# Optimization experiments

Measured on AMD Instinct MI355X. Metric: run time of the kernel, lower is better.

Reference implementation:

```python
import jax, jax.numpy as jnp
import numpy as np

B, S, HID = 2, 2048, 2048
H, KV, D = 32, 4, 128
G = H // KV
EPS = 1e-6
SCALE = D ** -0.5
ROPE_THETA = 1000000.0


def setup_inputs() -> dict:
    key = jax.random.key(0)
    ks = jax.random.split(key, 6)
    hidden_states = jax.random.normal(ks[0], (B, S, HID), jnp.float32)
    # real RoPE tables (position_embeddings passed into forward)
    inv_freq = 1.0 / (ROPE_THETA ** (np.arange(0, D, 2, dtype=np.float32) / D))
    ang = np.arange(S, dtype=np.float32)[:, None] * inv_freq[None, :]  # [S, D/2]
    emb = np.concatenate([ang, ang], axis=-1)  # [S, D]
    cos = jnp.broadcast_to(jnp.asarray(np.cos(emb)), (B, S, D))
    sin = jnp.broadcast_to(jnp.asarray(np.sin(emb)), (B, S, D))
    sd = 0.02
    wq = jax.random.normal(ks[1], (H * D, HID), jnp.float32) * sd
    wk = jax.random.normal(ks[2], (KV * D, HID), jnp.float32) * sd
    wv = jax.random.normal(ks[3], (KV * D, HID), jnp.float32) * sd
    wo = jax.random.normal(ks[4], (HID, H * D), jnp.float32) * sd
    q_norm_w = jnp.ones((D,), jnp.float32)
    k_norm_w = jnp.ones((D,), jnp.float32)
    return {"hidden_states": hidden_states, "cos": cos, "sin": sin,
            "wq": wq, "wk": wk, "wv": wv, "wo": wo,
            "q_norm_w": q_norm_w, "k_norm_w": k_norm_w}


def _rms_norm(x, w):
    var = jnp.mean(jnp.square(x), axis=-1, keepdims=True)
    return x * jax.lax.rsqrt(var + EPS) * w


def _rotate_half(x):
    x1, x2 = jnp.split(x, 2, axis=-1)
    return jnp.concatenate([-x2, x1], axis=-1)


def _rope(x, cos, sin):
    # x: [B,S,N,D]; cos/sin: [B,S,1,D] (unsqueeze_dim=2)
    return x * cos + _rotate_half(x) * sin


def reference(hidden_states, cos, sin, wq, wk, wv, wo, q_norm_w, k_norm_w):
    x = hidden_states
    q = jnp.einsum('bsh,oh->bso', x, wq).reshape(B, S, H, D)
    k = jnp.einsum('bsh,oh->bso', x, wk).reshape(B, S, KV, D)
    v = jnp.einsum('bsh,oh->bso', x, wv).reshape(B, S, KV, D)
    q = _rms_norm(q, q_norm_w)
    k = _rms_norm(k, k_norm_w)
    c = cos[:, :, None, :]
    s = sin[:, :, None, :]
    q = _rope(q, c, s)
    k = _rope(k, c, s)
    # GQA causal attention, BSND layout
    qg = q.reshape(B, S, KV, G, D)
    scores = jnp.einsum('bqkgd,bskd->bkgqs', qg, k) * SCALE  # [B,KV,G,Sq,Sk]
    causal = jnp.tril(jnp.ones((S, S), bool))
    scores = jnp.where(causal, scores, jnp.finfo(scores.dtype).min)
    p = jax.nn.softmax(scores, axis=-1)
    out = jnp.einsum('bkgqs,bskd->bqkgd', p, v).reshape(B, S, H * D)
    return jnp.einsum('bso,ho->bsh', out, wo)
```

## Files before the change

### kernel.cpp

```cpp
#include <hip/hip_runtime.h>
#include <hip/hip_bf16.h>

typedef __attribute__((ext_vector_type(8))) short short8;
typedef __attribute__((ext_vector_type(4))) float f32x4;

#define DEVI static __device__ __forceinline__

constexpr int Bb = 2, Ss = 2048, Hh = 32, KVc = 4, Dc = 128;
constexpr float EPSc = 1e-6f;
constexpr float SCALEc = 0.08838834764831845f;

DEVI float bf2f(short s) {
  unsigned u = ((unsigned)(unsigned short)s) << 16;
  float f; __builtin_memcpy(&f, &u, 4); return f;
}
DEVI short f2bf(float f) {
  __hip_bfloat16 h = __float2bfloat16(f);
  unsigned short u; __builtin_memcpy(&u, &h, 2); return (short)u;
}

#define GLDS(gsrc, ldst) __builtin_amdgcn_global_load_lds( \
    (const __attribute__((address_space(1))) void*)(gsrc), \
    (__attribute__((address_space(3))) void*)(ldst), 16, 0, 0)

struct Cvt5 { const float* src[5]; short* dst[5]; };
__global__ void cvt_all(Cvt5 a) {
  constexpr int CUM[6] = {0, 2097152, 4194304, 4456448, 4718592, 6815744};
  const int stride = gridDim.x * blockDim.x;
  for (int i = blockIdx.x * blockDim.x + threadIdx.x; i < 6815744; i += stride) {
    int s = 0;
#pragma unroll
    for (int t = 1; t < 5; ++t) if (i >= CUM[t]) s = t;
    int j = i - CUM[s];
    float4 v = ((const float4*)a.src[s])[j];
    short4 o;
    o.x = f2bf(v.x); o.y = f2bf(v.y); o.z = f2bf(v.z); o.w = f2bf(v.w);
    ((short4*)a.dst[s])[j] = o;
  }
}

template<int MODE>
__launch_bounds__(256, 2)
__global__ void gemm_bt(const short* __restrict__ A,
                        const short* __restrict__ B0,
                        const short* __restrict__ B1,
                        const short* __restrict__ B2,
                        short* __restrict__ oq,
                        short* __restrict__ ok,
                        short* __restrict__ ov,
                        float* __restrict__ of,
                        const float* __restrict__ cosb,
                        const float* __restrict__ sinb,
                        const float* __restrict__ qnw,
                        const float* __restrict__ knw,
                        int K)
{
  __shared__ short lA[128 * 32];
  __shared__ short lB[128 * 32];
  const int tid = threadIdx.x;
  const int lane = tid & 63;
  const int wvi = tid >> 6;
  const int l15 = lane & 15, g = lane >> 4;
  const int m0 = blockIdx.x * 128;
  const int nt = blockIdx.y;
  const short* Bp; int n0, region;
  if (MODE == 0) {
    if (nt < 32)      { Bp = B0; n0 = nt * 128;        region = 0; }
    else if (nt < 36) { Bp = B1; n0 = (nt - 32) * 128; region = 1; }
    else              { Bp = B2; n0 = (nt - 36) * 128; region = 2; }
  } else { Bp = B0; n0 = nt * 128; region = 3; }

  const int wrow = wvi * 32;
  const int srow = tid >> 2, schunk = tid & 3;

  f32x4 acc[2][8] = {};

  for (int k0 = 0; k0 < K; k0 += 32) {
    __syncthreads();
#pragma unroll
    for (int c = 0; c < 2; ++c) {
      int row = c * 64 + srow;
      int gc = schunk ^ ((row >> 1) & 3);
      GLDS(A  + (size_t)(m0 + row) * K + k0 + gc * 8, lA + (c * 256 + tid) * 8);
      GLDS(Bp + (size_t)(n0 + row) * K + k0 + gc * 8, lB + (c * 256 + tid) * 8);
    }
    __syncthreads();
    short8 afr[2], bfr[8];
#pragma unroll
    for (int i = 0; i < 2; ++i) {
      int ra = wrow + i * 16 + l15;
      afr[i] = *(const short8*)(lA + ra * 32 + ((g ^ ((ra >> 1) & 3)) * 8));
    }
#pragma unroll
    for (int i = 0; i < 8; ++i) {
      int rb = i * 16 + l15;
      bfr[i] = *(const short8*)(lB + rb * 32 + ((g ^ ((rb >> 1) & 3)) * 8));
    }
#pragma unroll
    for (int mi = 0; mi < 2; ++mi)
#pragma unroll
      for (int ni = 0; ni < 8; ++ni)
        acc[mi][ni] = __builtin_amdgcn_mfma_f32_16x16x32_bf16(afr[mi], bfr[ni], acc[mi][ni], 0, 0, 0);
  }

  if (MODE == 1) {
#pragma unroll
    for (int mi = 0; mi < 2; ++mi)
#pragma unroll
      for (int r = 0; r < 4; ++r) {
        int m = m0 + wrow + mi * 16 + g * 4 + r;
#pragma unroll
        for (int ni = 0; ni < 8; ++ni)
          of[(size_t)m * 2048 + n0 + ni * 16 + l15] = acc[mi][ni][r];
      }
  } else if (region == 2) {
#pragma unroll
    for (int mi = 0; mi < 2; ++mi)
#pragma unroll
      for (int r = 0; r < 4; ++r) {
        int m = m0 + wrow + mi * 16 + g * 4 + r;
        int b = m >> 11, s = m & 2047;
#pragma unroll
        for (int ni = 0; ni < 8; ++ni) {
          int n = n0 + ni * 16 + l15;
          int kvi = n >> 7, d = n & 127;
          ov[(((size_t)b * KVc + kvi) * 128 + d) * Ss + s] = f2bf(acc[mi][ni][r]);
        }
      }
  } else {
    const float* wnorm = (region == 0) ? qnw : knw;
    float w8[8];
#pragma unroll
    for (int ni = 0; ni < 8; ++ni) w8[ni] = wnorm[ni * 16 + l15];
#pragma unroll
    for (int mi = 0; mi < 2; ++mi)
#pragma unroll
      for (int r = 0; r < 4; ++r) {
        int m = m0 + wrow + mi * 16 + g * 4 + r;
        int b = m >> 11, s = m & 2047;
        float xv[8];
        float ssq = 0.f;
#pragma unroll
        for (int ni = 0; ni < 8; ++ni) { xv[ni] = acc[mi][ni][r]; ssq += xv[ni] * xv[ni]; }
        ssq += __shfl_xor(ssq, 1);
        ssq += __shfl_xor(ssq, 2);
        ssq += __shfl_xor(ssq, 4);
        ssq += __shfl_xor(ssq, 8);
        float inv = rsqrtf(ssq * (1.0f / 128.0f) + EPSc);
        float xn[8];
#pragma unroll
        for (int ni = 0; ni < 8; ++ni) xn[ni] = xv[ni] * inv * w8[ni];
        const float* cpr = cosb + ((size_t)b * Ss + s) * Dc;
        const float* spr = sinb + ((size_t)b * Ss + s) * Dc;
#pragma unroll
        for (int ni = 0; ni < 8; ++ni) {
          int dl = ni * 16 + l15;
          float c = cpr[dl], sn = spr[dl];
          float rot = (ni < 4) ? -xn[ni + 4] : xn[ni - 4];
          float o = xn[ni] * c + rot * sn;
          int n = n0 + dl;
          if (region == 0) {
            oq[(size_t)m * 4096 + n] = f2bf(o * SCALEc);
          } else {
            int kvi = n >> 7, d = n & 127;
            ok[(((size_t)b * KVc + kvi) * Ss + s) * 128 + d] = f2bf(o);
          }
        }
      }
  }
}

__launch_bounds__(256, 2)
__global__ void attn_fwd(const short* __restrict__ qb,
                         const short* __restrict__ kbuf,
                         const short* __restrict__ vtbuf,
                         short* __restrict__ ob)
{
  __shared__ short lK[2][64 * 128];
  __shared__ short lV[2][128 * 64];
  __shared__ short lP[4][32 * 32];
  const int tid = threadIdx.x, lane = tid & 63, wvi = tid >> 6;
  const int l15 = lane & 15, g = lane >> 4;
  const int pi = blockIdx.x, h = blockIdx.y, b = blockIdx.z;
  const int kv = h >> 3;
  const short* kp = kbuf  + ((size_t)b * KVc + kv) * Ss * 128;
  const short* vp = vtbuf + ((size_t)b * KVc + kv) * 128 * Ss;
  const int krow = tid >> 4, kch = tid & 15;
  const int vrow = tid >> 3, vch = tid & 7;

  for (int which = 0; which < 2; ++which) {
    const int qt = which ? (15 - pi) : pi;
    const int qwb = qt * 128 + wvi * 32;
    const int nkt = 2 * qt + 2;

    short8 qf[2][4];
#pragma unroll
    for (int qs = 0; qs < 2; ++qs)
#pragma unroll
      for (int dc = 0; dc < 4; ++dc)
        qf[qs][dc] = *(const short8*)(qb + (size_t)(b * Ss + qwb + qs * 16 + l15) * 4096
                                         + h * 128 + dc * 32 + g * 8);

    f32x4 oacc[2][8] = {};
    float mrun[2] = { -__builtin_inff(), -__builtin_inff() };
    float lrun[2] = { 0.f, 0.f };

    auto STAGE = [&](int kt, int bufi) {
      const int kb0 = kt * 64;
#pragma unroll
      for (int c = 0; c < 4; ++c) {
        int r = c * 16 + krow;
        int gc = kch ^ (r & 7);
        GLDS(kp + (size_t)(kb0 + r) * 128 + gc * 8, &lK[bufi][(c * 256 + tid) * 8]);
      }
#pragma unroll
      for (int c = 0; c < 4; ++c) {
        int r = c * 32 + vrow;
        int gc = vch ^ (r & 7);
        GLDS(vp + (size_t)r * Ss + kb0 + gc * 8, &lV[bufi][(c * 256 + tid) * 8]);
      }
    };

    STAGE(0, 0);
    STAGE(1, 1);

    for (int kt = 0; kt < nkt; ++kt) {
      const int cb = kt & 1;
      if (kt + 1 < nkt) asm volatile("s_waitcnt vmcnt(8)" ::: "memory");
      else              asm volatile("s_waitcnt vmcnt(0)" ::: "memory");
      __builtin_amdgcn_s_barrier();
      asm volatile("" ::: "memory");

#pragma unroll
      for (int half = 0; half < 2; ++half) {
        const int kb0 = kt * 64 + half * 32;
        if (kb0 <= qwb + 31) {
          short8 kf[2][4];
#pragma unroll
          for (int ks = 0; ks < 2; ++ks)
#pragma unroll
            for (int dc = 0; dc < 4; ++dc) {
              int row = half * 32 + ks * 16 + l15;
              kf[ks][dc] = *(const short8*)(&lK[cb][0] + row * 128 + (((dc * 4 + g) ^ (row & 7)) * 8));
            }
          f32x4 st[2][2] = {};
          __builtin_amdgcn_s_setprio(1);
#pragma unroll
          for (int qs = 0; qs < 2; ++qs)
#pragma unroll
            for (int ks = 0; ks < 2; ++ks)
#pragma unroll
              for (int dc = 0; dc < 4; ++dc)
                st[qs][ks] = __builtin_amdgcn_mfma_f32_16x16x32_bf16(kf[ks][dc], qf[qs][dc], st[qs][ks], 0, 0, 0);
          __builtin_amdgcn_s_setprio(0);

          const bool need_mask = (kb0 + 31 > qwb);
#pragma unroll
          for (int qs = 0; qs < 2; ++qs) {
            const int qg = qwb + qs * 16 + l15;
            float p[8];
            float tmax = -__builtin_inff();
#pragma unroll
            for (int ks = 0; ks < 2; ++ks)
#pragma unroll
              for (int r = 0; r < 4; ++r) {
                float v = st[qs][ks][r];
                if (need_mask && (kb0 + ks * 16 + g * 4 + r > qg)) v = -__builtin_inff();
                p[ks * 4 + r] = v;
                tmax = fmaxf(tmax, v);
              }
            tmax = fmaxf(tmax, __shfl_xor(tmax, 16));
            tmax = fmaxf(tmax, __shfl_xor(tmax, 32));
            float m_use = mrun[qs];
            if (__any(tmax > m_use + 8.0f)) {
              float mnew = fmaxf(m_use, tmax);
              float scl = __expf(m_use - mnew);
              lrun[qs] *= scl;
              mrun[qs] = mnew;
#pragma unroll
              for (int r = 0; r < 4; ++r) {
                float sc = __shfl(scl, g * 4 + r);
#pragma unroll
                for (int dt = 0; dt < 8; ++dt)
                  oacc[qs][dt][r] *= sc;
              }
              m_use = mnew;
            }
            float rsum = 0.f;
#pragma unroll
            for (int j = 0; j < 8; ++j) { p[j] = __expf(p[j] - m_use); rsum += p[j]; }
            rsum += __shfl_xor(rsum, 16);
            rsum += __shfl_xor(rsum, 32);
            lrun[qs] += rsum;
            {
              int row = qs * 16 + l15;
              int sw = (row >> 1) & 3;
              short* pr = lP[wvi] + row * 32;
#pragma unroll
              for (int ks = 0; ks < 2; ++ks) {
                int idx = (((2 * ks + (g >> 1)) ^ sw) * 8) + (g & 1) * 4;
                short4 pw;
                pw.x = f2bf(p[ks * 4 + 0]);
                pw.y = f2bf(p[ks * 4 + 1]);
                pw.z = f2bf(p[ks * 4 + 2]);
                pw.w = f2bf(p[ks * 4 + 3]);
                *(short4*)(pr + idx) = pw;
              }
            }
          }
          asm volatile("" ::: "memory");
          short8 vf[8];
#pragma unroll
          for (int dt = 0; dt < 8; ++dt) {
            int row = dt * 16 + l15;
            vf[dt] = *(const short8*)(&lV[cb][0] + row * 64 + (((half * 4 + g) ^ (row & 7)) * 8));
          }
          __builtin_amdgcn_s_setprio(1);
#pragma unroll
          for (int qs = 0; qs < 2; ++qs) {
            int row = qs * 16 + l15;
            short8 pf = *(const short8*)(lP[wvi] + row * 32 + ((g ^ ((row >> 1) & 3)) * 8));
#pragma unroll
            for (int dt = 0; dt < 8; ++dt)
              oacc[qs][dt] = __builtin_amdgcn_mfma_f32_16x16x32_bf16(pf, vf[dt], oacc[qs][dt], 0, 0, 0);
          }
          __builtin_amdgcn_s_setprio(0);
          asm volatile("" ::: "memory");
        }
      }

      asm volatile("" ::: "memory");
      __builtin_amdgcn_s_barrier();
      if (kt + 2 < nkt) STAGE(kt + 2, cb);
    }

#pragma unroll
    for (int qs = 0; qs < 2; ++qs)
#pragma unroll
      for (int r = 0; r < 4; ++r) {
        float inv = 1.0f / __shfl(lrun[qs], g * 4 + r);
        int qrow = qwb + qs * 16 + g * 4 + r;
        short* op = ob + (size_t)(b * Ss + qrow) * 4096 + h * 128;
#pragma unroll
        for (int dt = 0; dt < 8; ++dt)
          op[dt * 16 + l15] = f2bf(oacc[qs][dt][r] * inv);
      }
  }
}

extern "C" void kernel_launch(void* const* d_in, const int* in_sizes, int n_in,
                              void* d_out, int out_size, void* d_ws, size_t ws_size,
                              hipStream_t stream) {
  const float* x    = (const float*)d_in[0];
  const float* cosb = (const float*)d_in[1];
  const float* sinb = (const float*)d_in[2];
  const float* wq   = (const float*)d_in[3];
  const float* wk   = (const float*)d_in[4];
  const float* wv   = (const float*)d_in[5];
  const float* wo   = (const float*)d_in[6];
  const float* qw   = (const float*)d_in[7];
  const float* kw   = (const float*)d_in[8];

  size_t off = 0;
  auto alloc = [&](size_t bytes) {
    char* p = (char*)d_ws + off;
    off += (bytes + 255) & ~(size_t)255;
    return p;
  };
  short* x_bf  = (short*)alloc((size_t)8388608 * 2);
  short* wq_bf = (short*)alloc((size_t)8388608 * 2);
  short* wk_bf = (short*)alloc((size_t)1048576 * 2);
  short* wv_bf = (short*)alloc((size_t)1048576 * 2);
  short* wo_bf = (short*)alloc((size_t)8388608 * 2);
  short* q_bf  = (short*)alloc((size_t)16777216 * 2);
  short* k_bf  = (short*)alloc((size_t)2097152 * 2);
  short* v_bf  = (short*)alloc((size_t)2097152 * 2);
  short* ao_bf = (short*)alloc((size_t)16777216 * 2);

  Cvt5 ca;
  ca.src[0] = x;    ca.dst[0] = x_bf;
  ca.src[1] = wq;   ca.dst[1] = wq_bf;
  ca.src[2] = wk;   ca.dst[2] = wk_bf;
  ca.src[3] = wv;   ca.dst[3] = wv_bf;
  ca.src[4] = wo;   ca.dst[4] = wo_bf;
  cvt_all<<<2048, 256, 0, stream>>>(ca);

  gemm_bt<0><<<dim3(32, 40), 256, 0, stream>>>(x_bf, wq_bf, wk_bf, wv_bf,
                                               q_bf, k_bf, v_bf, nullptr,
                                               cosb, sinb, qw, kw, 2048);
  attn_fwd<<<dim3(8, 32, 2), 256, 0, stream>>>(q_bf, k_bf, v_bf, ao_bf);
  gemm_bt<1><<<dim3(32, 16), 256, 0, stream>>>(ao_bf, wo_bf, nullptr, nullptr,
                                               nullptr, nullptr, nullptr, (float*)d_out,
                                               nullptr, nullptr, nullptr, nullptr, 4096);
}
```

Before: 355.0 us.

## Double-buffer GEMM LDS tiles with async global-to-LDS prefetch two stages ahead

The projection GEMM kernel now keeps two LDS buffers for the A and B tiles and issues global_load_lds for the next K-slices while MFMAs run on the current one. Explicit vmcnt waits and raw barriers replace the two __syncthreads per iteration, so load latency can overlap with compute. The launch-bounds occupancy hint also rises from 2 to 4 blocks, which doubles LDS use per block and may force register spills. The hand-written vmcnt counting is fragile if the compiler emits other vector memory operations inside the loop.

```diff
diff --git a/kernel.cpp b/kernel.cpp
--- a/kernel.cpp
+++ b/kernel.cpp
@@ -40,7 +40,7 @@
 }
 
 template<int MODE>
-__launch_bounds__(256, 2)
+__launch_bounds__(256, 4)
 __global__ void gemm_bt(const short* __restrict__ A,
                         const short* __restrict__ B0,
                         const short* __restrict__ B1,
@@ -55,8 +55,8 @@
                         const float* __restrict__ knw,
                         int K)
 {
-  __shared__ short lA[128 * 32];
-  __shared__ short lB[128 * 32];
+  __shared__ short lA[2][128 * 32];
+  __shared__ short lB[2][128 * 32];
   const int tid = threadIdx.x;
   const int lane = tid & 63;
   const int wvi = tid >> 6;
@@ -75,32 +75,48 @@
 
   f32x4 acc[2][8] = {};
 
-  for (int k0 = 0; k0 < K; k0 += 32) {
-    __syncthreads();
+  auto STAGE = [&](int ks, int bufi) {
+    const int k0 = ks * 32;
 #pragma unroll
     for (int c = 0; c < 2; ++c) {
       int row = c * 64 + srow;
       int gc = schunk ^ ((row >> 1) & 3);
-      GLDS(A  + (size_t)(m0 + row) * K + k0 + gc * 8, lA + (c * 256 + tid) * 8);
-      GLDS(Bp + (size_t)(n0 + row) * K + k0 + gc * 8, lB + (c * 256 + tid) * 8);
+      GLDS(A  + (size_t)(m0 + row) * K + k0 + gc * 8, &lA[bufi][(c * 256 + tid) * 8]);
+      GLDS(Bp + (size_t)(n0 + row) * K + k0 + gc * 8, &lB[bufi][(c * 256 + tid) * 8]);
     }
-    __syncthreads();
+  };
+
+  const int nks = K >> 5;
+  STAGE(0, 0);
+  STAGE(1, 1);
+
+  for (int ks = 0; ks < nks; ++ks) {
+    const int cb = ks & 1;
+    if (ks + 1 < nks) asm volatile("s_waitcnt vmcnt(4)" ::: "memory");
+    else              asm volatile("s_waitcnt vmcnt(0)" ::: "memory");
+    __builtin_amdgcn_s_barrier();
+    asm volatile("" ::: "memory");
+
     short8 afr[2], bfr[8];
 #pragma unroll
     for (int i = 0; i < 2; ++i) {
       int ra = wrow + i * 16 + l15;
-      afr[i] = *(const short8*)(lA + ra * 32 + ((g ^ ((ra >> 1) & 3)) * 8));
+      afr[i] = *(const short8*)(&lA[cb][0] + ra * 32 + ((g ^ ((ra >> 1) & 3)) * 8));
     }
 #pragma unroll
     for (int i = 0; i < 8; ++i) {
       int rb = i * 16 + l15;
-      bfr[i] = *(const short8*)(lB + rb * 32 + ((g ^ ((rb >> 1) & 3)) * 8));
+      bfr[i] = *(const short8*)(&lB[cb][0] + rb * 32 + ((g ^ ((rb >> 1) & 3)) * 8));
     }
 #pragma unroll
     for (int mi = 0; mi < 2; ++mi)
 #pragma unroll
       for (int ni = 0; ni < 8; ++ni)
         acc[mi][ni] = __builtin_amdgcn_mfma_f32_16x16x32_bf16(afr[mi], bfr[ni], acc[mi][ni], 0, 0, 0);
+
+    asm volatile("" ::: "memory");
+    __builtin_amdgcn_s_barrier();
+    if (ks + 2 < nks) STAGE(ks + 2, cb);
   }
 
   if (MODE == 1) {
```

New measurement: 353.4 us. About the same (-0.4%).

## Rewrite projection GEMMs as 8-wave double-buffered pipelined kernels with larger tiles

Applied to the files above, without the earlier changes.

Replaces the simple single-buffered 128x128 GEMM with an 8-wave kernel that uses 256x256 (QKV) or 128x256 (output) tiles, BK=64, and double-buffered LDS. Global-to-LDS loads for the next K-slice are interleaved with MFMA phases, using s_setprio and vmcnt gating to overlap memory with compute. The V epilogue now writes packed short4 stores. The aim is to hide load latency and raise data reuse per tile, at the cost of much more LDS per block, which can reduce occupancy, and of fewer blocks on the grid.

```diff
diff --git a/kernel.cpp b/kernel.cpp
--- a/kernel.cpp
+++ b/kernel.cpp
@@ -40,103 +40,166 @@
 }
 
 template<int MODE>
-__launch_bounds__(256, 2)
-__global__ void gemm_bt(const short* __restrict__ A,
-                        const short* __restrict__ B0,
-                        const short* __restrict__ B1,
-                        const short* __restrict__ B2,
-                        short* __restrict__ oq,
-                        short* __restrict__ ok,
-                        short* __restrict__ ov,
-                        float* __restrict__ of,
-                        const float* __restrict__ cosb,
-                        const float* __restrict__ sinb,
-                        const float* __restrict__ qnw,
-                        const float* __restrict__ knw,
-                        int K)
+__launch_bounds__(512, 2)
+__global__ void gemm8(const short* __restrict__ A,
+                      const short* __restrict__ B0,
+                      const short* __restrict__ B1,
+                      const short* __restrict__ B2,
+                      short* __restrict__ oq,
+                      short* __restrict__ ok,
+                      short* __restrict__ ov,
+                      float* __restrict__ of,
+                      const float* __restrict__ cosb,
+                      const float* __restrict__ sinb,
+                      const float* __restrict__ qnw,
+                      const float* __restrict__ knw,
+                      int K)
 {
-  __shared__ short lA[128 * 32];
-  __shared__ short lB[128 * 32];
-  const int tid = threadIdx.x;
-  const int lane = tid & 63;
+  constexpr int BM   = (MODE == 0) ? 256 : 128;
+  constexpr int HBM  = BM / 2;
+  constexpr int NREP = (MODE == 0) ? 8 : 4;
+  constexpr int HNF  = NREP / 2;
+  constexpr int SA   = (MODE == 0) ? 2 : 1;
+  constexpr int SB   = 2;
+  constexpr int GATE = SA + SB;
+
+  __shared__ short lA[2][BM * 64];
+  __shared__ short lB[2][256 * 64];
+
+  const int tid = threadIdx.x, lane = tid & 63;
   const int wvi = tid >> 6;
   const int l15 = lane & 15, g = lane >> 4;
-  const int m0 = blockIdx.x * 128;
-  const int nt = blockIdx.y;
+  const int wm = (MODE == 0) ? (wvi >> 1) : (wvi >> 2);
+  const int wn = (MODE == 0) ? (wvi & 1) : (wvi & 3);
+  const int m0 = blockIdx.x * BM;
+  const int by = blockIdx.y;
   const short* Bp; int n0, region;
   if (MODE == 0) {
-    if (nt < 32)      { Bp = B0; n0 = nt * 128;        region = 0; }
-    else if (nt < 36) { Bp = B1; n0 = (nt - 32) * 128; region = 1; }
-    else              { Bp = B2; n0 = (nt - 36) * 128; region = 2; }
-  } else { Bp = B0; n0 = nt * 128; region = 3; }
-
-  const int wrow = wvi * 32;
-  const int srow = tid >> 2, schunk = tid & 3;
-
-  f32x4 acc[2][8] = {};
-
-  for (int k0 = 0; k0 < K; k0 += 32) {
-    __syncthreads();
-#pragma unroll
-    for (int c = 0; c < 2; ++c) {
-      int row = c * 64 + srow;
-      int gc = schunk ^ ((row >> 1) & 3);
-      GLDS(A  + (size_t)(m0 + row) * K + k0 + gc * 8, lA + (c * 256 + tid) * 8);
-      GLDS(Bp + (size_t)(n0 + row) * K + k0 + gc * 8, lB + (c * 256 + tid) * 8);
+    if (by < 16)      { Bp = B0; n0 = by * 256;        region = 0; }
+    else if (by < 18) { Bp = B1; n0 = (by - 16) * 256; region = 1; }
+    else              { Bp = B2; n0 = (by - 18) * 256; region = 2; }
+  } else { Bp = B0; n0 = by * 256; region = 3; }
+
+  f32x4 acc[4][NREP] = {};
+
+  auto stA = [&](int half, int slot, int kt) {
+#pragma unroll
+    for (int j = 0; j < SA; ++j) {
+      int rr = j * 64 + (tid >> 3);
+      int grow = ((rr >> 5) << 6) + half * 32 + (rr & 31);
+      GLDS(A + (size_t)(m0 + grow) * K + kt * 64 + (((tid & 7) ^ (rr & 7)) << 3),
+           &lA[slot][(half * HBM + j * 64) * 64 + tid * 8]);
     }
-    __syncthreads();
-    short8 afr[2], bfr[8];
-#pragma unroll
-    for (int i = 0; i < 2; ++i) {
-      int ra = wrow + i * 16 + l15;
-      afr[i] = *(const short8*)(lA + ra * 32 + ((g ^ ((ra >> 1) & 3)) * 8));
+  };
+  auto stB = [&](int half, int slot, int kt) {
+#pragma unroll
+    for (int j = 0; j < SB; ++j) {
+      int rr = j * 64 + (tid >> 3);
+      int gn = (MODE == 0) ? (((rr >> 6) << 7) + half * 64 + (rr & 63))
+                           : (((rr >> 5) << 6) + half * 32 + (rr & 31));
+      GLDS(Bp + (size_t)(n0 + gn) * K + kt * 64 + (((tid & 7) ^ (rr & 7)) << 3),
+           &lB[slot][(half * 128 + j * 64) * 64 + tid * 8]);
     }
-#pragma unroll
-    for (int i = 0; i < 8; ++i) {
-      int rb = i * 16 + l15;
-      bfr[i] = *(const short8*)(lB + rb * 32 + ((g ^ ((rb >> 1) & 3)) * 8));
+  };
+
+#define PH(SLOT, MH, NH, STG, GT) do {                                          \
+    short8 afr[2][2], bfr[HNF][2];                                              \
+    _Pragma("unroll")                                                           \
+    for (int mi2 = 0; mi2 < 2; ++mi2) {                                         \
+      int rp = (MH) * HBM + wm * 32 + mi2 * 16 + l15;                           \
+      _Pragma("unroll")                                                         \
+      for (int kk = 0; kk < 2; ++kk)                                            \
+        afr[mi2][kk] = *(const short8*)(&lA[SLOT][rp * 64 +                     \
+                         (((kk * 4 + g) ^ (rp & 7)) << 3)]);                    \
+    }                                                                           \
+    _Pragma("unroll")                                                           \
+    for (int nj = 0; nj < HNF; ++nj) {                                          \
+      int rp = (NH) * 128 + wn * (HNF * 16) + nj * 16 + l15;                    \
+      _Pragma("unroll")                                                         \
+      for (int kk = 0; kk < 2; ++kk)                                            \
+        bfr[nj][kk] = *(const short8*)(&lB[SLOT][rp * 64 +                      \
+                         (((kk * 4 + g) ^ (rp & 7)) << 3)]);                    \
+    }                                                                           \
+    STG;                                                                        \
+    asm volatile("" ::: "memory");                                              \
+    __builtin_amdgcn_s_barrier();                                               \
+    __builtin_amdgcn_s_setprio(1);                                              \
+    _Pragma("unroll")                                                           \
+    for (int mi2 = 0; mi2 < 2; ++mi2)                                           \
+      _Pragma("unroll")                                                         \
+      for (int nj = 0; nj < HNF; ++nj)                                          \
+        _Pragma("unroll")                                                       \
+        for (int kk = 0; kk < 2; ++kk)                                          \
+          acc[(MH)*2 + mi2][(NH)*HNF + nj] =                                    \
+            __builtin_amdgcn_mfma_f32_16x16x32_bf16(afr[mi2][kk], bfr[nj][kk],  \
+                acc[(MH)*2 + mi2][(NH)*HNF + nj], 0, 0, 0);                     \
+    __builtin_amdgcn_s_setprio(0);                                              \
+    GT;                                                                         \
+    asm volatile("" ::: "memory");                                              \
+    __builtin_amdgcn_s_barrier();                                               \
+  } while (0)
+
+  const int nks = K >> 6;
+  const int nit = nks >> 1;
+
+  stA(0, 0, 0); stB(0, 0, 0); stA(1, 0, 0); stB(1, 0, 0);
+  stA(0, 1, 1); stB(0, 1, 1);
+  asm volatile("s_waitcnt vmcnt(%0)" :: "n"(GATE) : "memory");
+  __builtin_amdgcn_s_barrier();
+
+  for (int it = 0; it < nit; ++it) {
+    const int kt1 = 2 * it + 1;
+    const int k2 = 2 * it + 2, k3 = 2 * it + 3;
+    const bool pre = (it + 1 < nit);
+    PH(0, 0, 0, { stA(1, 1, kt1); }, {});
+    PH(0, 0, 1, { stB(1, 1, kt1); }, {});
+    PH(0, 1, 0, { if (pre) stA(0, 0, k2); }, {});
+    PH(0, 1, 1, { if (pre) stB(0, 0, k2); },
+               { if (pre) asm volatile("s_waitcnt vmcnt(%0)" :: "n"(GATE) : "memory");
+                 else     asm volatile("s_waitcnt vmcnt(0)" ::: "memory"); });
+    PH(1, 0, 0, { if (pre) stA(1, 0, k2); }, {});
+    PH(1, 0, 1, { if (pre) stB(1, 0, k2); }, {});
+    PH(1, 1, 0, { if (pre) stA(0, 1, k3); }, {});
+    PH(1, 1, 1, { if (pre) stB(0, 1, k3); },
+               { if (pre) asm volatile("s_waitcnt vmcnt(%0)" :: "n"(GATE) : "memory"); });
+  }
+#undef PH
+
+  if (MODE == 1) {
+#pragma unroll
+    for (int mi = 0; mi < 4; ++mi)
+#pragma unroll
+      for (int r = 0; r < 4; ++r) {
+        int m = m0 + wm * 64 + mi * 16 + g * 4 + r;
+#pragma unroll
+        for (int ni = 0; ni < NREP; ++ni)
+          of[(size_t)m * 2048 + n0 + wn * (NREP * 16) + ni * 16 + l15] = acc[mi][ni][r];
+      }
+  } else if (region == 2) {
+    const int kvi = (by - 18) * 2 + wn;
+#pragma unroll
+    for (int mi = 0; mi < 4; ++mi) {
+      int mbase = m0 + wm * 64 + mi * 16 + g * 4;
+      int b = mbase >> 11, s0 = mbase & 2047;
+#pragma unroll
+      for (int ni = 0; ni < 8; ++ni) {
+        int d = ni * 16 + l15;
+        short4 pw;
+        pw.x = f2bf(acc[mi][ni][0]); pw.y = f2bf(acc[mi][ni][1]);
+        pw.z = f2bf(acc[mi][ni][2]); pw.w = f2bf(acc[mi][ni][3]);
+        *(short4*)(ov + (((size_t)b * KVc + kvi) * 128 + d) * Ss + s0) = pw;
+      }
     }
-#pragma unroll
-    for (int mi = 0; mi < 2; ++mi)
-#pragma unroll
-      for (int ni = 0; ni < 8; ++ni)
-        acc[mi][ni] = __builtin_amdgcn_mfma_f32_16x16x32_bf16(afr[mi], bfr[ni], acc[mi][ni], 0, 0, 0);
-  }
-
-  if (MODE == 1) {
-#pragma unroll
-    for (int mi = 0; mi < 2; ++mi)
-#pragma unroll
-      for (int r = 0; r < 4; ++r) {
-        int m = m0 + wrow + mi * 16 + g * 4 + r;
-#pragma unroll
-        for (int ni = 0; ni < 8; ++ni)
-          of[(size_t)m * 2048 + n0 + ni * 16 + l15] = acc[mi][ni][r];
-      }
-  } else if (region == 2) {
-#pragma unroll
-    for (int mi = 0; mi < 2; ++mi)
-#pragma unroll
-      for (int r = 0; r < 4; ++r) {
-        int m = m0 + wrow + mi * 16 + g * 4 + r;
-        int b = m >> 11, s = m & 2047;
-#pragma unroll
-        for (int ni = 0; ni < 8; ++ni) {
-          int n = n0 + ni * 16 + l15;
-          int kvi = n >> 7, d = n & 127;
-          ov[(((size_t)b * KVc + kvi) * 128 + d) * Ss + s] = f2bf(acc[mi][ni][r]);
-        }
-      }
   } else {
     const float* wnorm = (region == 0) ? qnw : knw;
     float w8[8];
 #pragma unroll
     for (int ni = 0; ni < 8; ++ni) w8[ni] = wnorm[ni * 16 + l15];
 #pragma unroll
-    for (int mi = 0; mi < 2; ++mi)
+    for (int mi = 0; mi < 4; ++mi)
 #pragma unroll
       for (int r = 0; r < 4; ++r) {
-        int m = m0 + wrow + mi * 16 + g * 4 + r;
+        int m = m0 + wm * 64 + mi * 16 + g * 4 + r;
         int b = m >> 11, s = m & 2047;
         float xv[8];
         float ssq = 0.f;
@@ -154,15 +217,14 @@
         const float* spr = sinb + ((size_t)b * Ss + s) * Dc;
 #pragma unroll
         for (int ni = 0; ni < 8; ++ni) {
-          int dl = ni * 16 + l15;
-          float c = cpr[dl], sn = spr[dl];
+          int d = ni * 16 + l15;
+          float c = cpr[d], sn = spr[d];
           float rot = (ni < 4) ? -xn[ni + 4] : xn[ni - 4];
           float o = xn[ni] * c + rot * sn;
-          int n = n0 + dl;
           if (region == 0) {
-            oq[(size_t)m * 4096 + n] = f2bf(o * SCALEc);
+            oq[(size_t)m * 4096 + n0 + wn * 128 + d] = f2bf(o * SCALEc);
           } else {
-            int kvi = n >> 7, d = n & 127;
+            int kvi = (by - 16) * 2 + wn;
             ok[(((size_t)b * KVc + kvi) * Ss + s) * 128 + d] = f2bf(o);
           }
         }
@@ -385,11 +447,11 @@
   ca.src[4] = wo;   ca.dst[4] = wo_bf;
   cvt_all<<<2048, 256, 0, stream>>>(ca);
 
-  gemm_bt<0><<<dim3(32, 40), 256, 0, stream>>>(x_bf, wq_bf, wk_bf, wv_bf,
-                                               q_bf, k_bf, v_bf, nullptr,
-                                               cosb, sinb, qw, kw, 2048);
+  gemm8<0><<<dim3(16, 20), 512, 0, stream>>>(x_bf, wq_bf, wk_bf, wv_bf,
+                                             q_bf, k_bf, v_bf, nullptr,
+                                             cosb, sinb, qw, kw, 2048);
   attn_fwd<<<dim3(8, 32, 2), 256, 0, stream>>>(q_bf, k_bf, v_bf, ao_bf);
-  gemm_bt<1><<<dim3(32, 16), 256, 0, stream>>>(ao_bf, wo_bf, nullptr, nullptr,
-                                               nullptr, nullptr, nullptr, (float*)d_out,
-                                               nullptr, nullptr, nullptr, nullptr, 4096);
-}
+  gemm8<1><<<dim3(32, 8), 512, 0, stream>>>(ao_bf, wo_bf, nullptr, nullptr,
+                                            nullptr, nullptr, nullptr, (float*)d_out,
+                                            nullptr, nullptr, nullptr, nullptr, 4096);
+}
```

New measurement: 388.5 us. +9.4%, slower.
